# Kernel optimization log

Measured on AMD Instinct MI355X. Metric: run time of the kernel, lower is better.

Reference implementation:

```python
import jax, jax.numpy as jnp
import numpy as np
from jax import lax

STRIDES = (8, 16, 32, 64, 128)
NUM_CLASSES = 80
NUM_CONVS = 4
C = 256
GROUPS = 32
EPS = 1e-5
SCORE_TH = 0.05
TOPK = 1000
NMS_TH = 0.6
MAX_DET = 100
FEAT_SHAPES = [(2, 256, 100, 152), (2, 256, 50, 76), (2, 256, 25, 38), (2, 256, 13, 19), (2, 256, 7, 10)]


def setup_inputs() -> dict:
    key = jax.random.key(0)
    ks = jax.random.split(key, 12)
    d = {}
    for i, shp in enumerate(FEAT_SHAPES):
        d[f"feat{i}"] = jax.random.normal(ks[i], shp, dtype=jnp.float32)
    d["cls_w"] = jax.random.normal(ks[5], (NUM_CONVS, C, C, 3, 3), dtype=jnp.float32) * 0.01
    d["cls_b"] = jnp.zeros((NUM_CONVS, C), jnp.float32)
    d["cls_gn_s"] = jnp.ones((NUM_CONVS, C), jnp.float32)
    d["cls_gn_b"] = jnp.zeros((NUM_CONVS, C), jnp.float32)
    d["box_w"] = jax.random.normal(ks[6], (NUM_CONVS, C, C, 3, 3), dtype=jnp.float32) * 0.01
    d["box_b"] = jnp.zeros((NUM_CONVS, C), jnp.float32)
    d["box_gn_s"] = jnp.ones((NUM_CONVS, C), jnp.float32)
    d["box_gn_b"] = jnp.zeros((NUM_CONVS, C), jnp.float32)
    d["score_w"] = jax.random.normal(ks[7], (NUM_CLASSES, C, 3, 3), dtype=jnp.float32) * 0.01
    d["score_b"] = jnp.zeros((NUM_CLASSES,), jnp.float32)  # prior_prob=0.5 -> bias 0
    d["bbox_w"] = jax.random.normal(ks[8], (4, C, 3, 3), dtype=jnp.float32) * 0.01
    d["bbox_b"] = jnp.zeros((4,), jnp.float32)
    d["ctr_w"] = jax.random.normal(ks[9], (1, C, 3, 3), dtype=jnp.float32) * 0.01
    d["ctr_b"] = jnp.zeros((1,), jnp.float32)
    d["scales"] = jnp.ones((5,), jnp.float32)
    return d


def conv3(x, w, b):
    y = lax.conv_general_dilated(x, w, (1, 1), ((1, 1), (1, 1)),
                                 dimension_numbers=("NCHW", "OIHW", "NCHW"))
    return y + b[None, :, None, None]


def groupnorm(x, s, b):
    n, c, h, w = x.shape
    xg = x.reshape(n, GROUPS, c // GROUPS, h, w)
    mu = xg.mean((2, 3, 4), keepdims=True)
    var = ((xg - mu) ** 2).mean((2, 3, 4), keepdims=True)
    xn = ((xg - mu) * lax.rsqrt(var + EPS)).reshape(n, c, h, w)
    return xn * s[None, :, None, None] + b[None, :, None, None]


def _subnet(x, ws, bs, gss, gbs):
    for i in range(NUM_CONVS):
        x = jax.nn.relu(groupnorm(conv3(x, ws[i], bs[i]), gss[i], gbs[i]))
    return x


def _nms_single(bxs, scs, cls_i):
    # bxs (M,4), scs (M,), cls_i (M,) int32. class-aware NMS via coordinate offset.
    cls_f = cls_i.astype(bxs.dtype)
    obxs = bxs + (cls_f * 1e4)[:, None]
    areas = jnp.maximum(obxs[:, 2] - obxs[:, 0], 0.) * jnp.maximum(obxs[:, 3] - obxs[:, 1], 0.)
    idxs = jnp.arange(scs.shape[0])

    def body(s, _):
        i = jnp.argmax(s)
        si = s[i]
        bi = bxs[i]
        ob = obxs[i]
        iw = jnp.maximum(jnp.minimum(ob[2], obxs[:, 2]) - jnp.maximum(ob[0], obxs[:, 0]), 0.)
        ih = jnp.maximum(jnp.minimum(ob[3], obxs[:, 3]) - jnp.maximum(ob[1], obxs[:, 1]), 0.)
        inter = iw * ih
        iou = inter / jnp.maximum(areas[i] + areas - inter, 1e-6)
        valid = si > 0.
        s_new = jnp.where(valid, jnp.where((iou > NMS_TH) | (idxs == i), 0., s), s)
        row = jnp.concatenate([bi, jnp.stack([si, cls_f[i]])]) * valid.astype(bxs.dtype)
        return s_new, row

    _, out = lax.scan(body, scs, None, length=MAX_DET)
    return out  # (MAX_DET, 6): x1,y1,x2,y2,score,class


def _forward(feats, cls_w, cls_b, cls_gn_s, cls_gn_b, box_w, box_b, box_gn_s, box_gn_b,
             score_w, score_b, bbox_w, bbox_b, ctr_w, ctr_b, scales):
    all_boxes, all_scores, all_classes = [], [], []
    for l, f in enumerate(feats):
        cls_t = _subnet(f, cls_w, cls_b, cls_gn_s, cls_gn_b)
        box_t = _subnet(f, box_w, box_b, box_gn_s, box_gn_b)
        logits = conv3(cls_t, score_w, score_b)                      # (N,K,H,W)
        reg = jax.nn.relu(scales[l] * conv3(box_t, bbox_w, bbox_b))  # (N,4,H,W)
        ctr = conv3(cls_t, ctr_w, ctr_b)                             # (N,1,H,W) centerness_on_cls
        n, k, h, w = logits.shape
        logits = logits.reshape(n, k, h * w).transpose(0, 2, 1)      # (N,HW,K)
        reg = reg.reshape(n, 4, h * w).transpose(0, 2, 1)            # (N,HW,4)
        ctr = ctr.reshape(n, 1, h * w).transpose(0, 2, 1)            # (N,HW,1)
        stride = float(STRIDES[l])
        xs = (jnp.arange(w, dtype=jnp.float32) + 0.5) * stride
        ys = (jnp.arange(h, dtype=jnp.float32) + 0.5) * stride
        px = jnp.broadcast_to(xs[None, :], (h, w)).reshape(-1)
        py = jnp.broadcast_to(ys[:, None], (h, w)).reshape(-1)
        boxes = jnp.stack([px - reg[..., 0] * stride, py - reg[..., 1] * stride,
                           px + reg[..., 2] * stride, py + reg[..., 3] * stride], axis=-1)
        scores = jnp.sqrt(jax.nn.sigmoid(logits) * jax.nn.sigmoid(ctr))  # (N,HW,K)
        flat = scores.reshape(n, -1)
        kk = min(TOPK, flat.shape[1])
        topv, topi = lax.top_k(flat, kk)
        anchor_i = topi // k
        class_i = topi % k
        lvl_boxes = jnp.take_along_axis(boxes, anchor_i[..., None], axis=1)  # (N,kk,4)
        topv = jnp.where(topv > SCORE_TH, topv, 0.)
        all_boxes.append(lvl_boxes)
        all_scores.append(topv)
        all_classes.append(class_i)
    cb = jnp.concatenate(all_boxes, axis=1)
    cs = jnp.concatenate(all_scores, axis=1)
    cc = jnp.concatenate(all_classes, axis=1)
    return jax.vmap(_nms_single)(cb, cs, cc)  # (N, MAX_DET, 6)


def reference(feat0, feat1, feat2, feat3, feat4, cls_w, cls_b, cls_gn_s, cls_gn_b,
              box_w, box_b, box_gn_s, box_gn_b, score_w, score_b, bbox_w, bbox_b,
              ctr_w, ctr_b, scales):
    feats = [feat0, feat1, feat2, feat3, feat4]
    return _forward(feats, cls_w, cls_b, cls_gn_s, cls_gn_b, box_w, box_b, box_gn_s, box_gn_b,
                    score_w, score_b, bbox_w, bbox_b, ctr_w, ctr_b, scales)
```

## Files before the change

### kernel.cpp

```cpp
#include <hip/hip_runtime.h>
#include <math.h>


#define KCLS 80
#define TOPKK 1000
#define NCAND 5000
#define MAXDET 100
#define TOTHW 20267

constexpr int cHa[5]  = {100, 50, 25, 13, 7};
constexpr int cWa[5]  = {152, 76, 38, 19, 10};
constexpr int cHWa[5] = {15200, 3800, 950, 247, 70};
constexpr int cPa[5]  = {0, 15200, 19000, 19950, 20197};
constexpr int cTXa[5] = {19, 10, 5, 3, 2};
constexpr int cPTa[5] = {0, 247, 317, 337, 343};
constexpr int cTa[5]  = {247, 70, 20, 6, 2};
constexpr float cSa[5] = {8.f, 16.f, 32.f, 64.f, 128.f};
constexpr int cPCh[5] = {0, 238, 298, 313, 317};

typedef _Float16 h8 __attribute__((ext_vector_type(8)));
typedef float f4 __attribute__((ext_vector_type(4)));

struct FeatPtrs { const float* p[5]; };

__device__ __forceinline__ int lvl_of_tile(int bx) {
  return (bx < 247) ? 0 : (bx < 317) ? 1 : (bx < 337) ? 2 : (bx < 343) ? 3 : 4;
}
__device__ __forceinline__ int lvl_of_pix(int gi) {
  return (gi < 15200) ? 0 : (gi < 19000) ? 1 : (gi < 19950) ? 2 : (gi < 20197) ? 3 : 4;
}

__global__ __launch_bounds__(256) void k_tf(FeatPtrs fp, float* __restrict__ FT) {
  int b = blockIdx.x, n = blockIdx.y;
  int l = (b < 238) ? 0 : (b < 298) ? 1 : (b < 313) ? 2 : (b < 317) ? 3 : 4;
  int ch = b - cPCh[l];
  int HW = cHWa[l];
  int px0 = ch * 64;
  const float* src = fp.p[l] + (size_t)n * 256 * HW;
  __shared__ float tile[64][65];
  int tid = threadIdx.x;
  int a0 = tid & 63, a1 = tid >> 6;
  for (int icc = 0; icc < 256; icc += 64) {
    __syncthreads();
#pragma unroll
    for (int j = 0; j < 16; ++j) {
      int ic = icc + a1 * 16 + j;
      int px = px0 + a0;
      tile[a0][a1 * 16 + j] = (px < HW) ? src[(size_t)ic * HW + px] : 0.f;
    }
    __syncthreads();
#pragma unroll
    for (int j = 0; j < 16; ++j) {
      int pxl = a1 * 16 + j;
      int px = px0 + pxl;
      if (px < HW)
        FT[((size_t)(n * TOTHW + cPa[l] + px)) * 256 + icc + a0] = tile[pxl][a0];
    }
  }
}

__global__ void k_rep(const float* __restrict__ w, const float* __restrict__ w2,
                      _Float16* __restrict__ Wh, _Float16* __restrict__ Wl,
                      int OC, int OCpad) {
  int i = blockIdx.x * 256 + threadIdx.x;
  int tot = 2304 * OCpad;
  if (i >= tot) return;
  int j = i & 7, kh = (i >> 3) & 3, c = (i >> 5) & 15;
  int rest = i >> 9;
  int G = OCpad >> 4;
  int g = rest % G, ti = rest / G;
  int ics = ti & 7, t = ti >> 3;
  int oc = g * 16 + c, ic = ics * 32 + kh * 8 + j;
  float v = 0.f;
  if (oc < OC) v = w[((size_t)oc * 256 + ic) * 9 + t];
  else if (w2 != nullptr && oc == OC) v = w2[(size_t)ic * 9 + t];
  float sv = v * 2048.f;
  _Float16 h = (_Float16)sv;
  Wh[i] = h;
  Wl[i] = (_Float16)(sv - (float)h);
}

template<bool AFFINE, bool GN_PART, bool HEAD, int NT>
__global__ __launch_bounds__(256) void k_cmf(
    const float* __restrict__ actIn,
    const _Float16* __restrict__ Wh, const _Float16* __restrict__ Wl,
    const float* __restrict__ bias1, const float* __restrict__ bias2,
    const float* __restrict__ cab, float* __restrict__ out,
    int outCH, int OC, double* __restrict__ part) {
  const int bx = blockIdx.x;
  const int lvl = lvl_of_tile(bx);
  const int tile = bx - cPTa[lvl];
  const int H = cHa[lvl], W = cWa[lvl];
  const int tx0 = (tile % cTXa[lvl]) * 8, ty0 = (tile / cTXa[lvl]) * 8;
  const int n = blockIdx.z;
  const int t = threadIdx.x, wv = t >> 6, lane = t & 63;
  const int kh = lane >> 4, c = lane & 15;

  __shared__ _Float16 sH[6400];
  __shared__ _Float16 sL[6400];

  const float* cabL = cab + (size_t)(lvl * 2 + n) * 512;

  const float* sp[4];
  int shp[4], sgp[4];
  bool sinb[4], shas[4];
#pragma unroll
  for (int s = 0; s < 4; ++s) {
    int e = t + 256 * s;
    bool has = e < 800;
    int grp = e & 7, hp = e >> 3;
    if (hp > 99) hp = 99;
    int yy = hp / 10, xx = hp % 10;
    int gy = ty0 + yy - 1, gx = tx0 + xx - 1;
    bool inb = has && ((unsigned)gy < (unsigned)H) && ((unsigned)gx < (unsigned)W);
    int gpx = inb ? (cPa[lvl] + gy * W + gx) : 0;
    sp[s] = actIn + ((size_t)(n * TOTHW + gpx)) * 256 + grp * 8;
    shp[s] = hp; sgp[s] = grp; sinb[s] = inb; shas[s] = has;
  }

  f4 acc[4][NT];
#pragma unroll
  for (int m = 0; m < 4; ++m)
#pragma unroll
    for (int nt = 0; nt < NT; ++nt) acc[m][nt] = (f4)(0.f);

  float4 fv[4][2];
#pragma unroll
  for (int s = 0; s < 4; ++s) {
    if (sinb[s]) {
      fv[s][0] = *(const float4*)(sp[s]);
      fv[s][1] = *(const float4*)(sp[s] + 4);
    } else {
      fv[s][0] = make_float4(0.f, 0.f, 0.f, 0.f);
      fv[s][1] = make_float4(0.f, 0.f, 0.f, 0.f);
    }
  }

  const int lB = (c * 4 + kh) * 8;

#pragma unroll 1
  for (int icc = 0; icc < 256; icc += 64) {
    __syncthreads();
#pragma unroll
    for (int s = 0; s < 4; ++s) {
      if (shas[s]) {
        float vv[8];
        vv[0] = fv[s][0].x; vv[1] = fv[s][0].y; vv[2] = fv[s][0].z; vv[3] = fv[s][0].w;
        vv[4] = fv[s][1].x; vv[5] = fv[s][1].y; vv[6] = fv[s][1].z; vv[7] = fv[s][1].w;
        if (AFFINE && sinb[s]) {
#pragma unroll
          for (int j = 0; j < 8; ++j) {
            int ch = icc + sgp[s] * 8 + j;
            vv[j] = fmaxf(0.f, fmaf(vv[j], cabL[2 * ch], cabL[2 * ch + 1]));
          }
        }
        h8 hv, lv2;
#pragma unroll
        for (int j = 0; j < 8; ++j) {
          float sv = vv[j] * 32.f;
          _Float16 hh = (_Float16)sv;
          hv[j] = hh;
          lv2[j] = (_Float16)(sv - (float)hh);
        }
        int boff = ((shp[s] << 7) + (sgp[s] << 4)) ^ ((shp[s] & 7) << 4);
        *(h8*)((char*)sH + boff) = hv;
        *(h8*)((char*)sL + boff) = lv2;
      }
    }
    if (icc < 192) {
#pragma unroll
      for (int s = 0; s < 4; ++s) {
        if (sinb[s]) {
          fv[s][0] = *(const float4*)(sp[s] + icc + 64);
          fv[s][1] = *(const float4*)(sp[s] + icc + 68);
        }
      }
    }
    __syncthreads();

#pragma unroll 1
    for (int dy = 0; dy < 3; ++dy) {
#pragma unroll 1
      for (int dx = 0; dx < 3; ++dx) {
        const int t9 = dy * 3 + dx;
#pragma unroll
        for (int ics = 0; ics < 2; ++ics) {
          const int ICS = (icc >> 5) + ics;
          size_t wb = ((size_t)(t9 * 8 + ICS) * (NT * 4) + wv * NT) * 512 + lB;
          h8 bh[NT], bl[NT];
#pragma unroll
          for (int nt = 0; nt < NT; ++nt) {
            bh[nt] = *(const h8*)(Wh + wb + nt * 512);
            bl[nt] = *(const h8*)(Wl + wb + nt * 512);
          }
#pragma unroll
          for (int m = 0; m < 4; ++m) {
            int pxA = m * 16 + c;
            int hpA = ((pxA >> 3) + dy) * 10 + (pxA & 7) + dx;
            int boffA = ((hpA << 7) + (ics << 6) + (kh << 4)) ^ ((hpA & 7) << 4);
            h8 Ah = *(const h8*)((const char*)sH + boffA);
            h8 Al = *(const h8*)((const char*)sL + boffA);
#pragma unroll
            for (int nt = 0; nt < NT; ++nt) {
              acc[m][nt] = __builtin_amdgcn_mfma_f32_16x16x32_f16(Ah, bh[nt], acc[m][nt], 0, 0, 0);
              acc[m][nt] = __builtin_amdgcn_mfma_f32_16x16x32_f16(Ah, bl[nt], acc[m][nt], 0, 0, 0);
              acc[m][nt] = __builtin_amdgcn_mfma_f32_16x16x32_f16(Al, bh[nt], acc[m][nt], 0, 0, 0);
            }
          }
        }
      }
    }
  }

  const float inv = 1.f / 65536.f;
#pragma unroll
  for (int nt = 0; nt < NT; ++nt) {
    int oc = wv * (NT * 16) + nt * 16 + c;
    float bb;
    if (HEAD) bb = (oc < KCLS) ? bias1[oc] : (oc == KCLS ? bias2[0] : 0.f);
    else bb = (oc < OC) ? bias1[oc] : 0.f;
    double s = 0.0, ss = 0.0;
#pragma unroll
    for (int m = 0; m < 4; ++m) {
#pragma unroll
      for (int r = 0; r < 4; ++r) {
        int px = m * 16 + kh * 4 + r;
        int oy = ty0 + (px >> 3), ox = tx0 + (px & 7);
        bool vpx = (oy < H) && (ox < W);
        float y = fmaf(acc[m][nt][r], inv, bb);
        if (vpx && oc < OC)
          out[((size_t)(n * TOTHW + cPa[lvl] + oy * W + ox)) * outCH + oc] = y;
        if (GN_PART && vpx) { double d = (double)y; s += d; ss += d * d; }
      }
    }
    if (GN_PART) {
#pragma unroll
      for (int msk = 16; msk <= 32; msk <<= 1) {
        s += __shfl_xor(s, msk, 64);
        ss += __shfl_xor(ss, msk, 64);
      }
#pragma unroll
      for (int msk = 1; msk <= 4; msk <<= 1) {
        s += __shfl_xor(s, msk, 64);
        ss += __shfl_xor(ss, msk, 64);
      }
      if (lane == 0 || lane == 8) {
        int G = wv * 8 + nt * 2 + (lane >> 3);
        size_t sl = (((size_t)bx * 2 + n) * 32 + G) * 2;
        part[sl] = s;
        part[sl + 1] = ss;
      }
    }
  }
}

__global__ __launch_bounds__(256) void k_coef(const double* __restrict__ part,
                                              const float* __restrict__ gs,
                                              const float* __restrict__ gb,
                                              float* __restrict__ cab) {
  int l = blockIdx.x >> 6, ng = blockIdx.x & 63, n = ng >> 5, g = ng & 31;
  int T = cTa[l];
  double s = 0.0, ss = 0.0;
  for (int tt = threadIdx.x; tt < T; tt += 256) {
    size_t sl = (((size_t)(cPTa[l] + tt) * 2 + n) * 32 + g) * 2;
    s += part[sl]; ss += part[sl + 1];
  }
  __shared__ double rs[256], rss[256];
  rs[threadIdx.x] = s; rss[threadIdx.x] = ss;
  __syncthreads();
  for (int off = 128; off > 0; off >>= 1) {
    if (threadIdx.x < off) {
      rs[threadIdx.x] += rs[threadIdx.x + off];
      rss[threadIdx.x] += rss[threadIdx.x + off];
    }
    __syncthreads();
  }
  if (threadIdx.x == 0) {
    int len = 8 * cHWa[l];
    double mu = rs[0] / len;
    double var = rss[0] / len - mu * mu;
    double rsq = 1.0 / sqrt(var + 1e-5);
    for (int cc = 0; cc < 8; ++cc) {
      int ch = g * 8 + cc;
      double A = rsq * (double)gs[ch];
      cab[((size_t)(l * 2 + n) * 256 + ch) * 2] = (float)A;
      cab[((size_t)(l * 2 + n) * 256 + ch) * 2 + 1] = (float)((double)gb[ch] - mu * A);
    }
  }
}

__global__ void k_dscore(const float* __restrict__ LG, float* __restrict__ SF) {
  size_t i = (size_t)blockIdx.x * 256 + threadIdx.x;
  size_t tot = (size_t)2 * TOTHW * 80;
  if (i >= tot) return;
  int c = (int)(i % 80);
  size_t g = i / 80;
  const float* base = LG + g * 96;
  float lg = base[c];
  float ct = base[80];
  float s1 = 1.f / (1.f + expf(-lg));
  float s2 = 1.f / (1.f + expf(-ct));
  SF[i] = sqrtf(s1 * s2);
}

__global__ void k_dbox(const float* __restrict__ RG, const float* __restrict__ scales,
                       float* __restrict__ BX) {
  int i = blockIdx.x * 256 + threadIdx.x;
  if (i >= 2 * TOTHW) return;
  int gi = i % TOTHW;
  int l = lvl_of_pix(gi);
  int a = gi - cPa[l];
  int W = cWa[l];
  const float* rg = RG + (size_t)i * 8;
  float sc = scales[l];
  float stride = cSa[l];
  float r0 = fmaxf(0.f, sc * rg[0]);
  float r1 = fmaxf(0.f, sc * rg[1]);
  float r2 = fmaxf(0.f, sc * rg[2]);
  float r3 = fmaxf(0.f, sc * rg[3]);
  int x = a % W, yv = a / W;
  float px = (x + 0.5f) * stride, py = (yv + 0.5f) * stride;
  float* bp = BX + (size_t)i * 4;
  bp[0] = px - r0 * stride; bp[1] = py - r1 * stride;
  bp[2] = px + r2 * stride; bp[3] = py + r3 * stride;
}

__global__ void k_hist1(const float* __restrict__ SF, unsigned* __restrict__ hist) {
  int nl = blockIdx.y; int n = nl & 1, l = nl >> 1;
  const float* s = SF + ((size_t)n * TOTHW + cPa[l]) * 80;
  int M = cHWa[l] * 80;
  unsigned* h = hist + nl * 1024;
  __shared__ unsigned lh[1024];
  for (int i = threadIdx.x; i < 1024; i += blockDim.x) lh[i] = 0;
  __syncthreads();
  for (int i = blockIdx.x * blockDim.x + threadIdx.x; i < M; i += gridDim.x * blockDim.x) {
    unsigned key = __float_as_uint(s[i]);
    unsigned b = key >> 20; if (b > 1023u) b = 1023u;
    atomicAdd(&lh[b], 1u);
  }
  __syncthreads();
  for (int i = threadIdx.x; i < 1024; i += blockDim.x)
    if (lh[i]) atomicAdd(&h[i], lh[i]);
}

__global__ __launch_bounds__(256) void k_resolve1(const unsigned* __restrict__ hist,
                                                  unsigned* __restrict__ ctl) {
  int nl = blockIdx.x;
  const unsigned* h = hist + nl * 1024;
  int t = threadIdx.x;
  unsigned loc[4];
  unsigned chunk = 0;
#pragma unroll
  for (int j = 0; j < 4; ++j) { loc[j] = h[t * 4 + j]; chunk += loc[j]; }
  __shared__ unsigned csum[256];
  csum[t] = chunk;
  __syncthreads();
  for (int off = 1; off < 256; off <<= 1) {
    unsigned v = (t + off < 256) ? csum[t + off] : 0u;
    __syncthreads();
    csum[t] += v;
    __syncthreads();
  }
  unsigned above = csum[t] - chunk;
  unsigned sfx[5];
  sfx[4] = above;
#pragma unroll
  for (int j = 3; j >= 0; --j) sfx[j] = sfx[j + 1] + loc[j];
#pragma unroll
  for (int j = 0; j < 4; ++j) {
    if (sfx[j] >= TOPKK && sfx[j + 1] < TOPKK) {
      ctl[nl] = (unsigned)(t * 4 + j);
      ctl[10 + nl] = sfx[j + 1];
    }
  }
}

__global__ void k_hist2(const float* __restrict__ SF, const unsigned* __restrict__ ctl,
                        unsigned* __restrict__ hist2) {
  int nl = blockIdx.y; int n = nl & 1, l = nl >> 1;
  unsigned b1 = ctl[nl];
  const float* s = SF + ((size_t)n * TOTHW + cPa[l]) * 80;
  int M = cHWa[l] * 80;
  unsigned* h = hist2 + nl * 4096;
  __shared__ unsigned lh[4096];
  for (int i = threadIdx.x; i < 4096; i += blockDim.x) lh[i] = 0;
  __syncthreads();
  for (int i = blockIdx.x * blockDim.x + threadIdx.x; i < M; i += gridDim.x * blockDim.x) {
    unsigned key = __float_as_uint(s[i]);
    if ((key >> 20) == b1) atomicAdd(&lh[(key >> 8) & 0xFFFu], 1u);
  }
  __syncthreads();
  for (int i = threadIdx.x; i < 4096; i += blockDim.x)
    if (lh[i]) atomicAdd(&h[i], lh[i]);
}

__global__ __launch_bounds__(256) void k_resolve2(const unsigned* __restrict__ hist2,
                                                  const unsigned* __restrict__ ctlin,
                                                  unsigned* __restrict__ ctl) {
  int nl = blockIdx.x;
  const unsigned* h = hist2 + nl * 4096;
  unsigned b1 = ctlin[nl];
  unsigned m1 = ctlin[10 + nl];
  int t = threadIdx.x;
  unsigned loc[16];
  unsigned chunk = 0;
#pragma unroll
  for (int j = 0; j < 16; ++j) { loc[j] = h[t * 16 + j]; chunk += loc[j]; }
  __shared__ unsigned csum[256];
  csum[t] = chunk;
  __syncthreads();
  for (int off = 1; off < 256; off <<= 1) {
    unsigned v = (t + off < 256) ? csum[t + off] : 0u;
    __syncthreads();
    csum[t] += v;
    __syncthreads();
  }
  unsigned above = csum[t] - chunk;
  unsigned sfx[17];
  sfx[16] = above;
#pragma unroll
  for (int j = 15; j >= 0; --j) sfx[j] = sfx[j + 1] + loc[j];
#pragma unroll
  for (int j = 0; j < 16; ++j) {
    if (m1 + sfx[j] >= TOPKK && m1 + sfx[j + 1] < TOPKK)
      ctl[20 + nl] = (b1 << 12) | (unsigned)(t * 16 + j);
  }
}

__device__ __forceinline__ void write_cand(int n, int l, int pos, float v, int i,
                                           float* csc, float* ccl, int* gai) {
  int a = i / KCLS, c = i - a * KCLS;
  int g = n * NCAND + pos;
  csc[g] = (v > 0.05f) ? v : 0.f;
  ccl[g] = (float)c;
  gai[g] = cPa[l] + a;
}

__global__ void k_compact(const float* __restrict__ SF, const unsigned* __restrict__ ctl,
                          unsigned* __restrict__ cnt, float* __restrict__ eqV,
                          unsigned* __restrict__ eqI,
                          float* csc, float* ccl, int* gai) {
  int nl = blockIdx.y; int n = nl & 1, l = nl >> 1;
  const float* s = SF + ((size_t)n * TOTHW + cPa[l]) * 80;
  int M = cHWa[l] * 80;
  unsigned P = ctl[20 + nl];
  int loff = l * TOPKK;
  for (int i = blockIdx.x * blockDim.x + threadIdx.x; i < M; i += gridDim.x * blockDim.x) {
    float v = s[i];
    unsigned k24 = __float_as_uint(v) >> 8;
    if (k24 < P) continue;
    if (k24 > P) {
      unsigned slot = atomicAdd(&cnt[nl], 1u);
      write_cand(n, l, loff + (int)slot, v, i, csc, ccl, gai);
    } else {
      unsigned e = atomicAdd(&cnt[10 + nl], 1u);
      if (e < 2048u) { eqV[nl * 2048 + e] = v; eqI[nl * 2048 + e] = (unsigned)i; }
    }
  }
}

__global__ void k_eq(const float* __restrict__ eqV, const unsigned* __restrict__ eqI,
                     const unsigned* __restrict__ cnt,
                     float* csc, float* ccl, int* gai) {
  int nl = blockIdx.x; int n = nl & 1, l = nl >> 1;
  int above = (int)cnt[nl];
  unsigned ec = cnt[10 + nl];
  int E = ec < 2048u ? (int)ec : 2048;
  int r = TOPKK - above;
  int loff = l * TOPKK;
  for (int e = threadIdx.x; e < E; e += blockDim.x) {
    float v = eqV[nl * 2048 + e];
    unsigned idx = eqI[nl * 2048 + e];
    int rank = 0;
    for (int j = 0; j < E; ++j) {
      float vj = eqV[nl * 2048 + j];
      unsigned ij = eqI[nl * 2048 + j];
      if (vj > v || (vj == v && ij < idx)) rank++;
    }
    if (rank < r)
      write_cand(n, l, loff + above + rank, v, (int)idx, csc, ccl, gai);
  }
}

__global__ void k_gather(const int* __restrict__ gai, const float* __restrict__ ccl,
                         const float* __restrict__ BX,
                         float* __restrict__ cbx, float* __restrict__ cob) {
  int i = blockIdx.x * 256 + threadIdx.x;
  if (i >= 2 * NCAND) return;
  int n = i / NCAND;
  int a = gai[i];
  if (a < 0 || a >= TOTHW) a = 0;
  const float* bp = BX + ((size_t)n * TOTHW + a) * 4;
  float b0 = bp[0], b1 = bp[1], b2 = bp[2], b3 = bp[3];
  float off = ccl[i] * 1e4f;
  cbx[(size_t)i * 4 + 0] = b0; cbx[(size_t)i * 4 + 1] = b1;
  cbx[(size_t)i * 4 + 2] = b2; cbx[(size_t)i * 4 + 3] = b3;
  cob[(size_t)i * 4 + 0] = b0 + off; cob[(size_t)i * 4 + 1] = b1 + off;
  cob[(size_t)i * 4 + 2] = b2 + off; cob[(size_t)i * 4 + 3] = b3 + off;
}

__global__ __launch_bounds__(1024) void k_nms(
    const float* __restrict__ cbox, const float* __restrict__ cscore,
    const float* __restrict__ ccls, float* __restrict__ out) {
  const int n = blockIdx.x;
  const int tid = threadIdx.x;
  const int wid = tid >> 6, lane = tid & 63;
  __shared__ float redV[16];
  __shared__ int redJ[16];
  __shared__ float sOB[10];

  float sc[5], bxr[5][4], obr[5][4], ar[5], cl[5];
#pragma unroll
  for (int q = 0; q < 5; ++q) {
    int j = q * 1024 + tid;
    if (j < NCAND) {
      size_t g = (size_t)n * NCAND + j;
      sc[q] = cscore[g];
      float4 b = *(const float4*)(cbox + g * 4);
      float cc = ccls[g];
      float off = cc * 1e4f;
      cl[q] = cc;
      bxr[q][0] = b.x; bxr[q][1] = b.y; bxr[q][2] = b.z; bxr[q][3] = b.w;
      obr[q][0] = b.x + off; obr[q][1] = b.y + off;
      obr[q][2] = b.z + off; obr[q][3] = b.w + off;
      ar[q] = fmaxf(obr[q][2] - obr[q][0], 0.f) * fmaxf(obr[q][3] - obr[q][1], 0.f);
    } else {
      sc[q] = -1.f; cl[q] = 0.f;
      bxr[q][0] = bxr[q][1] = bxr[q][2] = bxr[q][3] = 0.f;
      obr[q][0] = 1e30f; obr[q][1] = 1e30f; obr[q][2] = -1e30f; obr[q][3] = -1e30f;
      ar[q] = 0.f;
    }
  }

  for (int it = 0; it < MAXDET; ++it) {
    float mv = sc[0]; int mj = tid;
#pragma unroll
    for (int q = 1; q < 5; ++q) {
      if (sc[q] > mv) { mv = sc[q]; mj = q * 1024 + tid; }
    }
#pragma unroll
    for (int off = 1; off < 64; off <<= 1) {
      float ov = __shfl_xor(mv, off);
      int oj = __shfl_xor(mj, off);
      if (ov > mv || (ov == mv && oj < mj)) { mv = ov; mj = oj; }
    }
    if (lane == 0) { redV[wid] = mv; redJ[wid] = mj; }
    __syncthreads();
    float bv = redV[0]; int bj = redJ[0];
#pragma unroll
    for (int w = 1; w < 16; ++w) {
      float v2 = redV[w]; int j2 = redJ[w];
      if (v2 > bv || (v2 == bv && j2 < bj)) { bv = v2; bj = j2; }
    }
    const bool owner = ((bj & 1023) == tid);
    if (owner) {
      int q = bj >> 10;
      sOB[0] = obr[q][0]; sOB[1] = obr[q][1]; sOB[2] = obr[q][2]; sOB[3] = obr[q][3];
      sOB[4] = ar[q];
      sOB[5] = bxr[q][0]; sOB[6] = bxr[q][1]; sOB[7] = bxr[q][2]; sOB[8] = bxr[q][3];
      sOB[9] = cl[q];
    }
    __syncthreads();
    const bool valid = bv > 0.f;
    if (valid) {
      float ox1 = sOB[0], oy1 = sOB[1], ox2 = sOB[2], oy2 = sOB[3], ai = sOB[4];
#pragma unroll
      for (int q = 0; q < 5; ++q) {
        int j = q * 1024 + tid;
        float iw = fmaxf(fminf(ox2, obr[q][2]) - fmaxf(ox1, obr[q][0]), 0.f);
        float ih = fmaxf(fminf(oy2, obr[q][3]) - fmaxf(oy1, obr[q][1]), 0.f);
        float inter = iw * ih;
        float iou = inter / fmaxf(ai + ar[q] - inter, 1e-6f);
        if (iou > 0.6f || j == bj) sc[q] = 0.f;
      }
      if (owner) {
        float* o = out + ((size_t)n * MAXDET + it) * 6;
        o[0] = sOB[5]; o[1] = sOB[6]; o[2] = sOB[7]; o[3] = sOB[8];
        o[4] = bv; o[5] = sOB[9];
      }
    } else if (tid == 0) {
      float* o = out + ((size_t)n * MAXDET + it) * 6;
      o[0] = o[1] = o[2] = o[3] = o[4] = o[5] = 0.f;
    }
  }
}

extern "C" void kernel_launch(void* const* d_in, const int* in_sizes, int n_in,
                              void* d_out, int out_size, void* d_ws, size_t ws_size,
                              hipStream_t stream) {
  FeatPtrs fp;
  for (int i = 0; i < 5; ++i) fp.p[i] = (const float*)d_in[i];
  const float* cls_w = (const float*)d_in[5];
  const float* cls_b = (const float*)d_in[6];
  const float* cls_gs = (const float*)d_in[7];
  const float* cls_gb = (const float*)d_in[8];
  const float* box_w = (const float*)d_in[9];
  const float* box_b = (const float*)d_in[10];
  const float* box_gs = (const float*)d_in[11];
  const float* box_gb = (const float*)d_in[12];
  const float* score_w = (const float*)d_in[13];
  const float* score_b = (const float*)d_in[14];
  const float* bbox_w = (const float*)d_in[15];
  const float* bbox_b = (const float*)d_in[16];
  const float* ctr_w = (const float*)d_in[17];
  const float* ctr_b = (const float*)d_in[18];
  const float* scales = (const float*)d_in[19];

  float* ws = (float*)d_ws;
  const size_t A_off    = 0;
  const size_t B_off    = 10376704;
  const size_t WTh_off  = 20753408;
  const size_t WTl_off  = 21933056;
  const size_t WSh_off  = 23112704;
  const size_t WSl_off  = 23260160;
  const size_t WBh_off  = 23407616;
  const size_t WBl_off  = 23481344;
  const size_t PART_off = 23555072;
  const size_t CAB_off  = 23731712;
  const size_t CSC_off  = 23736832;
  const size_t CCL_off  = 23746832;
  const size_t GAI_off  = 23756832;
  const size_t H1_off   = 23766832;
  const size_t H2_off   = 23777072;
  const size_t CNT_off  = 23818032;
  const size_t CTL_off  = 23818064;
  const size_t EQV_off  = 23818096;
  const size_t EQI_off  = 23838576;
  const size_t LG_off   = A_off + 0;
  const size_t SF_off   = A_off + 4000000;
  const size_t RG_off   = A_off + 7300000;
  const size_t BX_off   = A_off + 7700000;
  const size_t CBX_off  = A_off + 7900000;
  const size_t COB_off  = A_off + 7950000;

  float* A = ws + A_off;
  float* B = ws + B_off;
  _Float16* WTh = (_Float16*)(ws + WTh_off);
  _Float16* WTl = (_Float16*)(ws + WTl_off);
  _Float16* WSh = (_Float16*)(ws + WSh_off);
  _Float16* WSl = (_Float16*)(ws + WSl_off);
  _Float16* WBh = (_Float16*)(ws + WBh_off);
  _Float16* WBl = (_Float16*)(ws + WBl_off);
  double* PART = (double*)(ws + PART_off);
  float* CAB = ws + CAB_off;
  float* CSC = ws + CSC_off;
  float* CCL = ws + CCL_off;
  int* GAI = (int*)(ws + GAI_off);
  unsigned* H1 = (unsigned*)(ws + H1_off);
  unsigned* H2 = (unsigned*)(ws + H2_off);
  unsigned* CNT = (unsigned*)(ws + CNT_off);
  unsigned* CTL = (unsigned*)(ws + CTL_off);
  float* EQV = ws + EQV_off;
  unsigned* EQI = (unsigned*)(ws + EQI_off);
  float* LG = ws + LG_off;
  float* SF = ws + SF_off;
  float* RG = ws + RG_off;
  float* BX = ws + BX_off;
  float* CBX = ws + CBX_off;
  float* COB = ws + COB_off;

  hipMemsetAsync(CSC, 0, (CTL_off + 32 - CSC_off) * sizeof(float), stream);

  dim3 blk(256);
  for (int ll = 0; ll < 4; ++ll)
    hipLaunchKernelGGL(k_rep, dim3(2304), blk, 0, stream,
                       cls_w + (size_t)ll * 589824, (const float*)nullptr,
                       WTh + (size_t)ll * 589824, WTl + (size_t)ll * 589824, 256, 256);
  hipLaunchKernelGGL(k_rep, dim3(1152), blk, 0, stream, score_w, ctr_w, WSh, WSl, 80, 128);
  hipLaunchKernelGGL(k_rep, dim3(576), blk, 0, stream, bbox_w, (const float*)nullptr,
                     WBh, WBl, 4, 64);

  hipLaunchKernelGGL(k_tf, dim3(319, 2), blk, 0, stream, fp, B);

  dim3 gC(345, 1, 2);
  hipLaunchKernelGGL((k_cmf<false, true, false, 4>), gC, blk, 0, stream,
                     B, WTh, WTl, cls_b, (const float*)nullptr, CAB, A, 256, 256, PART);
  hipLaunchKernelGGL(k_coef, dim3(320), blk, 0, stream, PART, cls_gs, cls_gb, CAB);
  hipLaunchKernelGGL((k_cmf<true, true, false, 4>), gC, blk, 0, stream,
                     A, WTh + 589824, WTl + 589824, cls_b + 256, (const float*)nullptr, CAB, B, 256, 256, PART);
  hipLaunchKernelGGL(k_coef, dim3(320), blk, 0, stream, PART, cls_gs + 256, cls_gb + 256, CAB);
  hipLaunchKernelGGL((k_cmf<true, true, false, 4>), gC, blk, 0, stream,
                     B, WTh + 2 * 589824, WTl + 2 * 589824, cls_b + 512, (const float*)nullptr, CAB, A, 256, 256, PART);
  hipLaunchKernelGGL(k_coef, dim3(320), blk, 0, stream, PART, cls_gs + 512, cls_gb + 512, CAB);
  hipLaunchKernelGGL((k_cmf<true, true, false, 4>), gC, blk, 0, stream,
                     A, WTh + 3 * 589824, WTl + 3 * 589824, cls_b + 768, (const float*)nullptr, CAB, B, 256, 256, PART);
  hipLaunchKernelGGL(k_coef, dim3(320), blk, 0, stream, PART, cls_gs + 768, cls_gb + 768, CAB);

  hipLaunchKernelGGL((k_cmf<true, false, true, 2>), gC, blk, 0, stream,
                     B, WSh, WSl, score_b, ctr_b, CAB, LG, 96, 81, (double*)nullptr);

  hipLaunchKernelGGL(k_dscore, dim3(12667), blk, 0, stream, LG, SF);
  hipLaunchKernelGGL(k_hist1, dim3(128, 10), blk, 0, stream, SF, H1);
  hipLaunchKernelGGL(k_resolve1, dim3(10), blk, 0, stream, H1, CTL);
  hipLaunchKernelGGL(k_hist2, dim3(128, 10), blk, 0, stream, SF, CTL, H2);
  hipLaunchKernelGGL(k_resolve2, dim3(10), blk, 0, stream, H2, CTL, CTL);
  hipLaunchKernelGGL(k_compact, dim3(128, 10), blk, 0, stream, SF, CTL, CNT, EQV, EQI, CSC, CCL, GAI);
  hipLaunchKernelGGL(k_eq, dim3(10), blk, 0, stream, EQV, EQI, CNT, CSC, CCL, GAI);

  for (int ll = 0; ll < 4; ++ll)
    hipLaunchKernelGGL(k_rep, dim3(2304), blk, 0, stream,
                       box_w + (size_t)ll * 589824, (const float*)nullptr,
                       WTh + (size_t)ll * 589824, WTl + (size_t)ll * 589824, 256, 256);
  hipLaunchKernelGGL(k_tf, dim3(319, 2), blk, 0, stream, fp, B);

  hipLaunchKernelGGL((k_cmf<false, true, false, 4>), gC, blk, 0, stream,
                     B, WTh, WTl, box_b, (const float*)nullptr, CAB, A, 256, 256, PART);
  hipLaunchKernelGGL(k_coef, dim3(320), blk, 0, stream, PART, box_gs, box_gb, CAB);
  hipLaunchKernelGGL((k_cmf<true, true, false, 4>), gC, blk, 0, stream,
                     A, WTh + 589824, WTl + 589824, box_b + 256, (const float*)nullptr, CAB, B, 256, 256, PART);
  hipLaunchKernelGGL(k_coef, dim3(320), blk, 0, stream, PART, box_gs + 256, box_gb + 256, CAB);
  hipLaunchKernelGGL((k_cmf<true, true, false, 4>), gC, blk, 0, stream,
                     B, WTh + 2 * 589824, WTl + 2 * 589824, box_b + 512, (const float*)nullptr, CAB, A, 256, 256, PART);
  hipLaunchKernelGGL(k_coef, dim3(320), blk, 0, stream, PART, box_gs + 512, box_gb + 512, CAB);
  hipLaunchKernelGGL((k_cmf<true, true, false, 4>), gC, blk, 0, stream,
                     A, WTh + 3 * 589824, WTl + 3 * 589824, box_b + 768, (const float*)nullptr, CAB, B, 256, 256, PART);
  hipLaunchKernelGGL(k_coef, dim3(320), blk, 0, stream, PART, box_gs + 768, box_gb + 768, CAB);

  hipLaunchKernelGGL((k_cmf<true, false, false, 1>), gC, blk, 0, stream,
                     B, WBh, WBl, bbox_b, (const float*)nullptr, CAB, RG, 8, 4, (double*)nullptr);

  hipLaunchKernelGGL(k_dbox, dim3(159), blk, 0, stream, RG, scales, BX);
  hipLaunchKernelGGL(k_gather, dim3(40), blk, 0, stream, GAI, CCL, BX, CBX, COB);
  hipLaunchKernelGGL(k_nms, dim3(2), dim3(1024), 0, stream, CBX, CSC, CCL, (float*)d_out);
}
```

Before: 1.839 ms.

## Replace iterative block NMS with rank-sort, IoU bitmask matrix and serial walk

Replaces the single-block-per-image greedy NMS, which did 100 rounds of block-wide argmax with syncthreads, with three kernels. The first ranks candidates by score using an O(N^2) count and writes them in sorted order. The second builds a 64-bit suppression bitmask matrix in parallel across many blocks. The third walks the sorted list with one wavefront, picking the first surviving candidate via ffs and a shuffle-min and clearing suppressed bits. This trades per-iteration barriers and IoU recomputation for an upfront parallel IoU matrix of about 3.2MB per image, plus a quadratic ranking pass.

```diff
diff --git a/kernel.cpp b/kernel.cpp
--- a/kernel.cpp
+++ b/kernel.cpp
@@ -7,6 +7,7 @@
 #define NCAND 5000
 #define MAXDET 100
 #define TOTHW 20267
+#define TT 345
 
 constexpr int cHa[5]  = {100, 50, 25, 13, 7};
 constexpr int cWa[5]  = {152, 76, 38, 19, 10};
@@ -499,87 +500,109 @@
   cob[(size_t)i * 4 + 2] = b2 + off; cob[(size_t)i * 4 + 3] = b3 + off;
 }
 
-__global__ __launch_bounds__(1024) void k_nms(
-    const float* __restrict__ cbox, const float* __restrict__ cscore,
-    const float* __restrict__ ccls, float* __restrict__ out) {
-  const int n = blockIdx.x;
-  const int tid = threadIdx.x;
-  const int wid = tid >> 6, lane = tid & 63;
-  __shared__ float redV[16];
-  __shared__ int redJ[16];
-  __shared__ float sOB[10];
-
-  float sc[5], bxr[5][4], obr[5][4], ar[5], cl[5];
-#pragma unroll
-  for (int q = 0; q < 5; ++q) {
-    int j = q * 1024 + tid;
+__global__ __launch_bounds__(256) void k_rank(
+    const float* __restrict__ csc, const float* __restrict__ cob,
+    float* __restrict__ SSC, float* __restrict__ SAR,
+    int* __restrict__ SIDX, float4* __restrict__ SOX) {
+  int n = blockIdx.x / 20, seg = blockIdx.x % 20;
+  int i = seg * 256 + threadIdx.x;
+  bool act = i < NCAND;
+  float sci = act ? csc[(size_t)n * NCAND + i] : 0.f;
+  int rank = 0;
+  __shared__ float tj[256];
+  for (int jt = 0; jt < 20; ++jt) {
+    int j = jt * 256 + threadIdx.x;
+    tj[threadIdx.x] = (j < NCAND) ? csc[(size_t)n * NCAND + j] : -2.f;
+    __syncthreads();
+    if (act) {
+      for (int k = 0; k < 256; ++k) {
+        int jj = jt * 256 + k;
+        float v = tj[k];
+        rank += (v > sci || (v == sci && jj < i)) ? 1 : 0;
+      }
+    }
+    __syncthreads();
+  }
+  if (act) {
+    float4 b = *(const float4*)(cob + ((size_t)n * NCAND + i) * 4);
+    size_t r = (size_t)n * NCAND + rank;
+    SSC[r] = sci;
+    SAR[r] = fmaxf(b.z - b.x, 0.f) * fmaxf(b.w - b.y, 0.f);
+    SIDX[r] = i;
+    SOX[r] = b;
+  }
+}
+
+__global__ __launch_bounds__(256) void k_bmat(
+    const float4* __restrict__ SOX, const float* __restrict__ SAR,
+    unsigned long long* __restrict__ mat) {
+  int n = blockIdx.y;
+  int i = blockIdx.x * 4 + (threadIdx.x >> 6);
+  int lane = threadIdx.x & 63;
+  size_t base = (size_t)n * NCAND;
+  float4 bi = SOX[base + i];
+  float ai = SAR[base + i];
+  unsigned long long* row = mat + ((size_t)n * NCAND + i) * 80;
+  for (int c = i >> 6; c < 79; ++c) {
+    int j = c * 64 + lane;
+    bool bit = false;
     if (j < NCAND) {
-      size_t g = (size_t)n * NCAND + j;
-      sc[q] = cscore[g];
-      float4 b = *(const float4*)(cbox + g * 4);
-      float cc = ccls[g];
-      float off = cc * 1e4f;
-      cl[q] = cc;
-      bxr[q][0] = b.x; bxr[q][1] = b.y; bxr[q][2] = b.z; bxr[q][3] = b.w;
-      obr[q][0] = b.x + off; obr[q][1] = b.y + off;
-      obr[q][2] = b.z + off; obr[q][3] = b.w + off;
-      ar[q] = fmaxf(obr[q][2] - obr[q][0], 0.f) * fmaxf(obr[q][3] - obr[q][1], 0.f);
+      float4 bj = SOX[base + j];
+      float iw = fmaxf(fminf(bi.z, bj.z) - fmaxf(bi.x, bj.x), 0.f);
+      float ih = fmaxf(fminf(bi.w, bj.w) - fmaxf(bi.y, bj.y), 0.f);
+      float inter = iw * ih;
+      float iou = inter / fmaxf(ai + SAR[base + j] - inter, 1e-6f);
+      bit = (iou > 0.6f) || (j == i);
+    }
+    unsigned long long m = __ballot(bit);
+    if (lane == 0) row[c] = m;
+  }
+}
+
+__global__ __launch_bounds__(64) void k_walk(
+    const float* __restrict__ SSC, const int* __restrict__ SIDX,
+    const unsigned long long* __restrict__ mat,
+    const float* __restrict__ cbox, const float* __restrict__ ccls,
+    float* __restrict__ out) {
+  int n = blockIdx.x;
+  int l = threadIdx.x;
+  __shared__ float sS[NCAND];
+  __shared__ int pk[MAXDET];
+  __shared__ float pv[MAXDET];
+  for (int j = l; j < NCAND; j += 64) sS[j] = SSC[(size_t)n * NCAND + j];
+  unsigned long long a0 = ~0ull;
+  unsigned long long a1 = (l < 14) ? ~0ull : (l == 14 ? 0xFFull : 0ull);
+  __syncthreads();
+  for (int it = 0; it < MAXDET; ++it) {
+    int j0 = a0 ? (l * 64 + __ffsll((long long)a0) - 1) : (1 << 30);
+    int j1 = a1 ? ((64 + l) * 64 + __ffsll((long long)a1) - 1) : (1 << 30);
+    int loc = j0 < j1 ? j0 : j1;
+#pragma unroll
+    for (int off = 1; off < 64; off <<= 1) {
+      int o = __shfl_xor(loc, off);
+      loc = o < loc ? o : loc;
+    }
+    float bv = (loc < NCAND) ? sS[loc] : 0.f;
+    if (bv > 0.f) {
+      const unsigned long long* row = mat + ((size_t)n * NCAND + loc) * 80;
+      a0 &= ~row[l];
+      if (l < 15) a1 &= ~row[64 + l];
+      if (l == 0) { pk[it] = loc; pv[it] = bv; }
     } else {
-      sc[q] = -1.f; cl[q] = 0.f;
-      bxr[q][0] = bxr[q][1] = bxr[q][2] = bxr[q][3] = 0.f;
-      obr[q][0] = 1e30f; obr[q][1] = 1e30f; obr[q][2] = -1e30f; obr[q][3] = -1e30f;
-      ar[q] = 0.f;
-    }
-  }
-
-  for (int it = 0; it < MAXDET; ++it) {
-    float mv = sc[0]; int mj = tid;
-#pragma unroll
-    for (int q = 1; q < 5; ++q) {
-      if (sc[q] > mv) { mv = sc[q]; mj = q * 1024 + tid; }
-    }
-#pragma unroll
-    for (int off = 1; off < 64; off <<= 1) {
-      float ov = __shfl_xor(mv, off);
-      int oj = __shfl_xor(mj, off);
-      if (ov > mv || (ov == mv && oj < mj)) { mv = ov; mj = oj; }
-    }
-    if (lane == 0) { redV[wid] = mv; redJ[wid] = mj; }
-    __syncthreads();
-    float bv = redV[0]; int bj = redJ[0];
-#pragma unroll
-    for (int w = 1; w < 16; ++w) {
-      float v2 = redV[w]; int j2 = redJ[w];
-      if (v2 > bv || (v2 == bv && j2 < bj)) { bv = v2; bj = j2; }
-    }
-    const bool owner = ((bj & 1023) == tid);
-    if (owner) {
-      int q = bj >> 10;
-      sOB[0] = obr[q][0]; sOB[1] = obr[q][1]; sOB[2] = obr[q][2]; sOB[3] = obr[q][3];
-      sOB[4] = ar[q];
-      sOB[5] = bxr[q][0]; sOB[6] = bxr[q][1]; sOB[7] = bxr[q][2]; sOB[8] = bxr[q][3];
-      sOB[9] = cl[q];
-    }
-    __syncthreads();
-    const bool valid = bv > 0.f;
-    if (valid) {
-      float ox1 = sOB[0], oy1 = sOB[1], ox2 = sOB[2], oy2 = sOB[3], ai = sOB[4];
-#pragma unroll
-      for (int q = 0; q < 5; ++q) {
-        int j = q * 1024 + tid;
-        float iw = fmaxf(fminf(ox2, obr[q][2]) - fmaxf(ox1, obr[q][0]), 0.f);
-        float ih = fmaxf(fminf(oy2, obr[q][3]) - fmaxf(oy1, obr[q][1]), 0.f);
-        float inter = iw * ih;
-        float iou = inter / fmaxf(ai + ar[q] - inter, 1e-6f);
-        if (iou > 0.6f || j == bj) sc[q] = 0.f;
-      }
-      if (owner) {
-        float* o = out + ((size_t)n * MAXDET + it) * 6;
-        o[0] = sOB[5]; o[1] = sOB[6]; o[2] = sOB[7]; o[3] = sOB[8];
-        o[4] = bv; o[5] = sOB[9];
-      }
-    } else if (tid == 0) {
-      float* o = out + ((size_t)n * MAXDET + it) * 6;
+      if (l == 0) { pk[it] = -1; pv[it] = 0.f; }
+    }
+  }
+  __syncthreads();
+  for (int it = l; it < MAXDET; it += 64) {
+    float* o = out + ((size_t)n * MAXDET + it) * 6;
+    int p = pk[it];
+    if (p >= 0) {
+      int orig = SIDX[(size_t)n * NCAND + p];
+      size_t g = (size_t)n * NCAND + orig;
+      const float* bb = cbox + g * 4;
+      o[0] = bb[0]; o[1] = bb[1]; o[2] = bb[2]; o[3] = bb[3];
+      o[4] = pv[it]; o[5] = ccls[g];
+    } else {
       o[0] = o[1] = o[2] = o[3] = o[4] = o[5] = 0.f;
     }
   }
@@ -632,6 +655,11 @@
   const size_t BX_off   = A_off + 7700000;
   const size_t CBX_off  = A_off + 7900000;
   const size_t COB_off  = A_off + 7950000;
+  const size_t SSCs_off = A_off + 8000000;
+  const size_t SARs_off = A_off + 8010000;
+  const size_t SIDX_off = A_off + 8020000;
+  const size_t SOXs_off = A_off + 8030000;
+  const size_t MAT_off  = A_off + 8100000;
 
   float* A = ws + A_off;
   float* B = ws + B_off;
@@ -658,6 +686,11 @@
   float* BX = ws + BX_off;
   float* CBX = ws + CBX_off;
   float* COB = ws + COB_off;
+  float* SSCs = ws + SSCs_off;
+  float* SARs = ws + SARs_off;
+  int* SIDXs = (int*)(ws + SIDX_off);
+  float4* SOXs = (float4*)(ws + SOXs_off);
+  unsigned long long* MATp = (unsigned long long*)(ws + MAT_off);
 
   hipMemsetAsync(CSC, 0, (CTL_off + 32 - CSC_off) * sizeof(float), stream);
 
@@ -672,7 +705,7 @@
 
   hipLaunchKernelGGL(k_tf, dim3(319, 2), blk, 0, stream, fp, B);
 
-  dim3 gC(345, 1, 2);
+  dim3 gC(TT, 1, 2);
   hipLaunchKernelGGL((k_cmf<false, true, false, 4>), gC, blk, 0, stream,
                      B, WTh, WTl, cls_b, (const float*)nullptr, CAB, A, 256, 256, PART);
   hipLaunchKernelGGL(k_coef, dim3(320), blk, 0, stream, PART, cls_gs, cls_gb, CAB);
@@ -721,5 +754,8 @@
 
   hipLaunchKernelGGL(k_dbox, dim3(159), blk, 0, stream, RG, scales, BX);
   hipLaunchKernelGGL(k_gather, dim3(40), blk, 0, stream, GAI, CCL, BX, CBX, COB);
-  hipLaunchKernelGGL(k_nms, dim3(2), dim3(1024), 0, stream, CBX, CSC, CCL, (float*)d_out);
-}
+  hipLaunchKernelGGL(k_rank, dim3(40), blk, 0, stream, CSC, COB, SSCs, SARs, SIDXs, SOXs);
+  hipLaunchKernelGGL(k_bmat, dim3(1250, 2), blk, 0, stream, SOXs, SARs, MATp);
+  hipLaunchKernelGGL(k_walk, dim3(2), dim3(64), 0, stream, SSCs, SIDXs, MATp, CBX, CCL,
+                     (float*)d_out);
+}
```

After: 1.752 ms. 4.7% less time.
